# Optimization experiments

Hardware: AMD Instinct MI355X
Metric: run time of the kernel (lower is better)

The kernel has to match this reference:

```python
import jax, jax.numpy as jnp
import numpy as np

B, QH, QW = 16, 64, 64
KH, KW = 64, 64
H, D, DK, K, S = 8, 256, 32, 4, 1


def setup_inputs() -> dict:
    key = jax.random.key(0)
    ks = jax.random.split(key, 16)
    def lin(i, din, dout, wscale=1.0):
        w = jax.random.normal(ks[i], (din, dout), jnp.float32) * (wscale / np.sqrt(din))
        b = jax.random.normal(ks[i + 1], (dout,), jnp.float32) * 0.02
        return w, b
    Wq, bq = lin(0, D, D)
    Wb, bb = lin(2, D, D)
    Wk, bk = lin(4, D, D)
    Woff, boff = lin(6, D, 2 * H * K * S, wscale=0.1)  # small offsets keep samples near ref point
    WA, bA = lin(8, D, H * K * S)
    Wm, bm = lin(10, D, D)
    return dict(
        query=jax.random.normal(ks[12], (B, QH, QW, D), jnp.float32),
        keys=jax.random.normal(ks[13], (B, KH, KW, D), jnp.float32),
        ref_point=jax.random.uniform(ks[14], (B, QH, QW, 2), jnp.float32),
        src_query=jax.random.normal(ks[15], (B, QH, QW, D), jnp.float32),
        Wq=Wq, bq=bq, Wb=Wb, bb=bb, Wk=Wk, bk=bk,
        Woff=Woff, boff=boff, WA=WA, bA=bA, Wm=Wm, bm=bm)


def _bilinear_zeros(img, px, py):
    # img [N, Hs, Ws, C]; px, py pixel coords [N, K, QH, QW]
    # Matches torch F.grid_sample(mode='bilinear', padding_mode='zeros'):
    # each out-of-bounds corner contributes zero.
    N, Hs, Ws, _ = img.shape
    x0 = jnp.floor(px); y0 = jnp.floor(py)
    wx1 = px - x0; wy1 = py - y0
    n = jnp.arange(N)[:, None, None, None]
    def corner(xf, yf, w):
        xi = xf.astype(jnp.int32); yi = yf.astype(jnp.int32)
        valid = (xi >= 0) & (xi < Ws) & (yi >= 0) & (yi < Hs)
        v = img[n, jnp.clip(yi, 0, Hs - 1), jnp.clip(xi, 0, Ws - 1)]
        return v * (w * valid)[..., None]
    return (corner(x0, y0, (1 - wx1) * (1 - wy1)) + corner(x0 + 1, y0, wx1 * (1 - wy1))
            + corner(x0, y0 + 1, (1 - wx1) * wy1) + corner(x0 + 1, y0 + 1, wx1 * wy1))


def reference(query, keys, ref_point, src_query, Wq, bq, Wb, bb, Wk, bk,
              Woff, boff, WA, bA, Wm, bm):
    _ = query @ Wq + bq  # q_proj output is computed but unused in the original forward
    sq = src_query @ Wb + bb
    off = (sq @ Woff + boff).reshape(B, QH, QW, H, S, K, 2)
    off = off.transpose(0, 3, 4, 5, 1, 2, 6).reshape(B * H, S, K, QH, QW, 2)
    A = jax.nn.softmax((sq @ WA + bA).reshape(B, QH, QW, H, S * K), axis=-1)
    A = A.transpose(0, 3, 1, 2, 4).reshape(B * H, QH, QW, S, K)
    # k_proj on the (single-scale) key feature map -> per-head maps [B*H, KH, KW, DK]
    kf = (keys @ Wk + bk).reshape(B, KH, KW, H, DK).transpose(0, 3, 1, 2, 4).reshape(B * H, KH, KW, DK)
    # restore_scale then torch .repeat(h,1,1,1): flat index n -> batch n % B (faithful to original)
    rr = ref_point * jnp.array([KW - 1, KH - 1], jnp.float32)
    rr = jnp.tile(rr, (H, 1, 1, 1))  # [B*H, QH, QW, 2]
    samples = []
    for l in range(S):
        pts = rr[:, None] + off[:, l]                 # [B*H, K, QH, QW, 2]
        vgx = 2.0 * pts[..., 0] / max(KW - 1, 1) - 1.0
        vgy = 2.0 * pts[..., 1] / max(KH - 1, 1) - 1.0
        px = ((vgx + 1.0) * KW - 1.0) / 2.0           # grid_sample align_corners=False unnormalize
        py = ((vgy + 1.0) * KH - 1.0) / 2.0
        samples.append(_bilinear_zeros(kf, px, py))   # [B*H, K, QH, QW, DK]
    samp = jnp.stack(samples, axis=1)                 # [B*H, S, K, QH, QW, DK]
    feat = jnp.einsum('nskhwd,nhwsk->nhwd', samp, A)  # weighted sum over scales*points
    feat = feat.reshape(B, H, QH, QW, DK).transpose(0, 2, 3, 1, 4).reshape(B, QH, QW, D)
    return feat @ Wm + bm
```

## Files before the change

### kernel.cpp

```cpp
#include <hip/hip_runtime.h>
#include <hip/hip_bf16.h>

using bf16 = __hip_bfloat16;
typedef short bf16x8 __attribute__((ext_vector_type(8)));
typedef short s16x4 __attribute__((ext_vector_type(4)));
typedef float f32x4 __attribute__((ext_vector_type(4)));
typedef unsigned int u32x4 __attribute__((ext_vector_type(4)));

#define DD 256
#define MTOT 65536

static __device__ __forceinline__ short f2bs(float f) {
    bf16 h = __float2bfloat16(f);
    return *reinterpret_cast<short*>(&h);
}

static __device__ __forceinline__ void gll16(const void* g, void* l) {
    __builtin_amdgcn_global_load_lds(
        (const __attribute__((address_space(1))) unsigned int*)g,
        (__attribute__((address_space(3))) unsigned int*)l, 16, 0, 0);
}

static __device__ __forceinline__ int swz_idx(int n, int k) {
    return n * 256 + ((((k >> 3) ^ (n & 7)) << 3) | (k & 7));
}

__global__ __launch_bounds__(256) void k_setup(
    const float* __restrict__ Wk, const float* __restrict__ Wm,
    bf16* __restrict__ WkT, bf16* __restrict__ WmT,
    const float* __restrict__ Wb, const float* __restrict__ bb,
    const float* __restrict__ Woff, const float* __restrict__ boff,
    const float* __restrict__ WA, const float* __restrict__ bA,
    bf16* __restrict__ WCt, float* __restrict__ bc)
{
    __shared__ float colw[256];
    __shared__ float red[256];
    int bid = blockIdx.x, t = threadIdx.x;
    if (bid < 512) {
        int idx = bid * 256 + t;
        int which = idx >> 16, e = idx & 65535;
        int i = e >> 8, j = e & 255;
        const float* src = which == 0 ? Wk : Wm;
        bf16*        dst = which == 0 ? WkT : WmT;
        dst[swz_idx(j, i)] = __float2bfloat16(src[e]);
        return;
    }
    int j = bid - 512;
    float cw = (j < 64) ? Woff[t * 64 + j] : WA[t * 32 + (j - 64)];
    colw[t] = cw;
    red[t] = bb[t] * cw;
    __syncthreads();
    float v = 0.f;
    const float* wbrow = Wb + (size_t)t * 256;
#pragma unroll 8
    for (int i = 0; i < 256; ++i) v += wbrow[i] * colw[i];
    WCt[swz_idx(j, t)] = __float2bfloat16(v);
    for (int s = 128; s > 0; s >>= 1) {
        __syncthreads();
        if (t < s) red[t] += red[t + s];
    }
    if (t == 0) bc[j] = red[0] + ((j < 64) ? boff[j] : bA[j - 64]);
}

template <int NTW, int NCOLS>
static __device__ __forceinline__ void gemm_lds3(
    const float* __restrict__ Av, const bf16* __restrict__ BTswz,
    bf16* __restrict__ Bs, char* __restrict__ As,
    int row0, int tid, f32x4 (&acc)[2][NTW])
{
    const int wave = tid >> 6, lane = tid & 63;
    const int rg = wave >> 1, cg = wave & 1;
    const int rsub = lane & 15, kg = lane >> 4;
    constexpr int SB = NCOLS / 32;
    const int arow_l = lane >> 4;
    const int kb  = (lane & 15) * 4;
    const int g_l = (lane & 15) >> 1;
    const int sub = (lane & 15) & 1;

    f32x4 areg[4];
    auto loadA = [&](int s) {
#pragma unroll
        for (int c = 0; c < 4; ++c) {
            int row = wave * 16 + c * 4 + arow_l;
            areg[c] = *(const f32x4*)(Av + (size_t)(row0 + row) * DD + s * 64 + kb);
        }
    };
    auto writeA = [&](int buf) {
#pragma unroll
        for (int c = 0; c < 4; ++c) {
            int row = wave * 16 + c * 4 + arow_l;
            s16x4 p;
#pragma unroll
            for (int e = 0; e < 4; ++e) p[e] = f2bs(areg[c][e]);
            *(s16x4*)(As + buf * 8192 + row * 128 + ((g_l ^ (row & 7)) << 4) + sub * 8) = p;
        }
    };
    auto stageB = [&](int s) {
#pragma unroll
        for (int i = 0; i < SB; ++i) {
            int cc = wave * SB + i;
            int i16 = cc * 64 + lane;
            int n = i16 >> 3, lg = i16 & 7;
            gll16(BTswz + (size_t)n * 256 + s * 64 + lg * 8, (char*)Bs + (size_t)i16 * 16);
        }
    };

    loadA(0);
    asm volatile("s_waitcnt vmcnt(0)" ::: "memory");
    writeA(0);
    int cur = 0;
#pragma unroll
    for (int s = 0; s < 4; ++s) {
        stageB(s);
        __builtin_amdgcn_sched_barrier(0);
        if (s < 3) {
            loadA(s + 1);
            asm volatile("s_waitcnt vmcnt(4)" ::: "memory");
        } else {
            asm volatile("s_waitcnt vmcnt(0)" ::: "memory");
        }
        asm volatile("s_waitcnt lgkmcnt(0)" ::: "memory");
        __builtin_amdgcn_s_barrier();
#pragma unroll
        for (int kkl = 0; kkl < 2; ++kkl) {
            bf16x8 afr[2];
#pragma unroll
            for (int st = 0; st < 2; ++st) {
                int row = rg * 32 + st * 16 + rsub;
                int g = kkl * 4 + kg;
                afr[st] = *(const bf16x8*)(As + cur * 8192 + row * 128 + ((g ^ (row & 7)) << 4));
            }
            int lg = kkl * 4 + kg;
#pragma unroll
            for (int nt = 0; nt < NTW; ++nt) {
                int n = cg * (NTW * 16) + nt * 16 + rsub;
                bf16x8 b = *(const bf16x8*)((const char*)Bs + (size_t)n * 128 + ((lg ^ (n & 7)) << 4));
                acc[0][nt] = __builtin_amdgcn_mfma_f32_16x16x32_bf16(afr[0], b, acc[0][nt], 0, 0, 0);
                acc[1][nt] = __builtin_amdgcn_mfma_f32_16x16x32_bf16(afr[1], b, acc[1][nt], 0, 0, 0);
            }
        }
        if (s < 3) {
            asm volatile("s_waitcnt vmcnt(0)" ::: "memory");
            writeA(cur ^ 1);
        }
        asm volatile("s_waitcnt lgkmcnt(0)" ::: "memory");
        __builtin_amdgcn_s_barrier();
        cur ^= 1;
    }
}

template <int NTW, int NCOLS>
static __device__ __forceinline__ void gemm_lds2b(
    const bf16* __restrict__ Av, const bf16* __restrict__ BTswz,
    bf16* __restrict__ Bs, char* __restrict__ As,
    int row0, int tid, f32x4 (&acc)[2][NTW])
{
    const int wave = tid >> 6, lane = tid & 63;
    const int rg = wave >> 1, cg = wave & 1;
    const int rsub = lane & 15, kg = lane >> 4;
    constexpr int SB = NCOLS / 32;
    constexpr int SA = 2;
    constexpr int ABYTES = 8192;

    auto stageB = [&](int s) {
#pragma unroll
        for (int i = 0; i < SB; ++i) {
            int cc = wave * SB + i;
            int i16 = cc * 64 + lane;
            int n = i16 >> 3, lg = i16 & 7;
            gll16(BTswz + (size_t)n * 256 + s * 64 + lg * 8, (char*)Bs + (size_t)i16 * 16);
        }
    };
    auto stageA = [&](int s, int buf) {
#pragma unroll
        for (int i = 0; i < SA; ++i) {
            int cc = wave * 2 + i;
            int row = cc * 8 + (lane >> 3);
            int g = (lane & 7) ^ (row & 7);
            gll16(Av + (size_t)(row0 + row) * DD + s * 64 + g * 8,
                  As + (size_t)buf * ABYTES + cc * 1024 + lane * 16);
        }
    };

    stageA(0, 0);
    int cur = 0;
#pragma unroll
    for (int s = 0; s < 4; ++s) {
        stageB(s);
        __builtin_amdgcn_sched_barrier(0);
        if (s < 3) {
            stageA(s + 1, cur ^ 1);
            asm volatile("s_waitcnt vmcnt(%0)" :: "i"(SA) : "memory");
        } else {
            asm volatile("s_waitcnt vmcnt(0)" ::: "memory");
        }
        __builtin_amdgcn_s_barrier();
#pragma unroll
        for (int kkl = 0; kkl < 2; ++kkl) {
            bf16x8 afr[2];
#pragma unroll
            for (int st = 0; st < 2; ++st) {
                int row = rg * 32 + st * 16 + rsub;
                const char* base = As + cur * ABYTES + row * 128;
                int g = kkl * 4 + kg;
                afr[st] = *(const bf16x8*)(base + ((g ^ (row & 7)) << 4));
            }
            int lg = kkl * 4 + kg;
#pragma unroll
            for (int nt = 0; nt < NTW; ++nt) {
                int n = cg * (NTW * 16) + nt * 16 + rsub;
                bf16x8 b = *(const bf16x8*)((const char*)Bs + (size_t)n * 128 + ((lg ^ (n & 7)) << 4));
                acc[0][nt] = __builtin_amdgcn_mfma_f32_16x16x32_bf16(afr[0], b, acc[0][nt], 0, 0, 0);
                acc[1][nt] = __builtin_amdgcn_mfma_f32_16x16x32_bf16(afr[1], b, acc[1][nt], 0, 0, 0);
            }
        }
        asm volatile("s_waitcnt lgkmcnt(0)" ::: "memory");
        __builtin_amdgcn_s_barrier();
        cur ^= 1;
    }
}

__global__ __launch_bounds__(256) void k_offA(
    const float* __restrict__ src, const bf16* __restrict__ WCt, const float* __restrict__ bc,
    float* __restrict__ off_ws, float* __restrict__ A_ws)
{
    __shared__ __align__(16) bf16 Bs[96 * 64];
    __shared__ __align__(16) char As[2 * 8192];
    int tid = threadIdx.x, lane = tid & 63, wave = tid >> 6;
    int row0 = blockIdx.x * 64;
    f32x4 acc[2][3] = {};
    gemm_lds3<3, 96>(src, WCt, Bs, As, row0, tid, acc);
    int col = lane & 15;
    int jbase = (wave & 1) * 48;
    int rb = row0 + (wave >> 1) * 32 + ((lane >> 4) << 2);
#pragma unroll
    for (int mt = 0; mt < 2; ++mt) {
#pragma unroll
        for (int nt = 0; nt < 3; ++nt) {
            int j = jbase + nt * 16 + col;
            if (j < 64) {
                float bias = bc[j];
#pragma unroll
                for (int r = 0; r < 4; ++r) {
                    int m = rb + mt * 16 + r;
                    off_ws[(size_t)m * 64 + j] = acc[mt][nt][r] + bias;
                }
            } else {
                int ac = j - 64;
                float bias = bc[j];
#pragma unroll
                for (int r = 0; r < 4; ++r) {
                    int m = rb + mt * 16 + r;
                    float v  = acc[mt][nt][r] + bias;
                    float mx = fmaxf(v, __shfl_xor(v, 1));
                    mx       = fmaxf(mx, __shfl_xor(mx, 2));
                    float e  = __expf(v - mx);
                    float su = e + __shfl_xor(e, 1);
                    su      += __shfl_xor(su, 2);
                    A_ws[(size_t)m * 32 + ac] = e / su;
                }
            }
        }
    }
}

__global__ __launch_bounds__(256) void k_gemm_kf(
    const float* __restrict__ keys, const bf16* __restrict__ WkT,
    const float* __restrict__ bk, bf16* __restrict__ kf)
{
    __shared__ __align__(16) bf16 Bs[256 * 64];
    __shared__ __align__(16) char As[2 * 8192];
    int tid = threadIdx.x, lane = tid & 63, wave = tid >> 6;
    int row0 = blockIdx.x * 64;
    f32x4 acc[2][8] = {};
    gemm_lds3<8, 256>(keys, WkT, Bs, As, row0, tid, acc);
    int col = lane & 15;
    int jbase = (wave & 1) * 128;
    int rb = row0 + (wave >> 1) * 32 + ((lane >> 4) << 2);
#pragma unroll
    for (int mt = 0; mt < 2; ++mt)
#pragma unroll
        for (int nt = 0; nt < 8; ++nt) {
            int j = jbase + nt * 16 + col;
            float bias = bk[j];
#pragma unroll
            for (int r = 0; r < 4; ++r) {
                int m = rb + mt * 16 + r;
                size_t dst = (((size_t)(m >> 12) * 8 + (j >> 5)) * 4096 + (m & 4095)) * 32 + (j & 31);
                kf[dst] = __float2bfloat16(acc[mt][nt][r] + bias);
            }
        }
}

__global__ __launch_bounds__(256) void k_sample(
    const float* __restrict__ ref_point, const float* __restrict__ off_ws,
    const float* __restrict__ A_ws, const bf16* __restrict__ kf,
    bf16* __restrict__ feat, int blk0)
{
    int bid = blockIdx.x + blk0;
    int xcd = bid & 7, within = bid >> 3;
    int b = xcd * 2 + (within >> 9);
    int pixblk = within & 511;
    int t  = threadIdx.x;
    int q  = t >> 5;
    int h  = (t >> 2) & 7;
    int cg = t & 3;
    int m  = (b << 12) + pixblk * 8 + q;
    int pix = m & 4095;
    int rbatch = (b * 8 + h) & 15;
    const float* rp = ref_point + ((size_t)rbatch * 4096 + pix) * 2;
    float rx = rp[0] * 63.0f;
    float ry = rp[1] * 63.0f;
    const bf16* kfh = kf + ((size_t)(b * 8 + h) * 4096) * 32 + cg * 8;
    f32x4 o0 = *(const f32x4*)(off_ws + (size_t)m * 64 + h * 8);
    f32x4 o1 = *(const f32x4*)(off_ws + (size_t)m * 64 + h * 8 + 4);
    f32x4 av = *(const f32x4*)(A_ws  + (size_t)m * 32 + h * 4);
    float acc[8] = {};
#pragma unroll
    for (int k = 0; k < 4; ++k) {
        float ox = (k < 2) ? o0[2 * k] : o1[2 * k - 4];
        float oy = (k < 2) ? o0[2 * k + 1] : o1[2 * k - 3];
        float a  = av[k];
        float px = (rx + ox) * (64.0f / 63.0f) - 0.5f;
        float py = (ry + oy) * (64.0f / 63.0f) - 0.5f;
        float x0 = floorf(px), y0 = floorf(py);
        float wx1 = px - x0, wy1 = py - y0;
        int xi = (int)x0, yi = (int)y0;
        float ax0 = (1.f - wx1) * ((xi     >= 0 && xi     < 64) ? 1.f : 0.f);
        float ax1 = wx1         * ((xi + 1 >= 0 && xi + 1 < 64) ? 1.f : 0.f);
        float ay0 = (1.f - wy1) * ((yi     >= 0 && yi     < 64) ? a : 0.f);
        float ay1 = wy1         * ((yi + 1 >= 0 && yi + 1 < 64) ? a : 0.f);
        int xc0 = min(max(xi, 0), 63),      xc1 = min(max(xi + 1, 0), 63);
        int yc0 = min(max(yi, 0), 63) * 64, yc1 = min(max(yi + 1, 0), 63) * 64;
        float w00 = ax0 * ay0, w01 = ax1 * ay0, w10 = ax0 * ay1, w11 = ax1 * ay1;
        bf16x8 v00 = *(const bf16x8*)(kfh + (yc0 + xc0) * 32);
        bf16x8 v01 = *(const bf16x8*)(kfh + (yc0 + xc1) * 32);
        bf16x8 v10 = *(const bf16x8*)(kfh + (yc1 + xc0) * 32);
        bf16x8 v11 = *(const bf16x8*)(kfh + (yc1 + xc1) * 32);
        u32x4 u00 = __builtin_bit_cast(u32x4, v00);
        u32x4 u01 = __builtin_bit_cast(u32x4, v01);
        u32x4 u10 = __builtin_bit_cast(u32x4, v10);
        u32x4 u11 = __builtin_bit_cast(u32x4, v11);
#pragma unroll
        for (int d = 0; d < 4; ++d) {
            acc[2 * d]     += w00 * __uint_as_float(u00[d] << 16)
                            + w01 * __uint_as_float(u01[d] << 16)
                            + w10 * __uint_as_float(u10[d] << 16)
                            + w11 * __uint_as_float(u11[d] << 16);
            acc[2 * d + 1] += w00 * __uint_as_float(u00[d] & 0xffff0000u)
                            + w01 * __uint_as_float(u01[d] & 0xffff0000u)
                            + w10 * __uint_as_float(u10[d] & 0xffff0000u)
                            + w11 * __uint_as_float(u11[d] & 0xffff0000u);
        }
    }
    bf16x8 o;
#pragma unroll
    for (int e = 0; e < 8; ++e) o[e] = f2bs(acc[e]);
    *(bf16x8*)(feat + (size_t)m * DD + h * 32 + cg * 8) = o;
}

__global__ __launch_bounds__(256) void k_gemm_out(
    const bf16* __restrict__ feat, const bf16* __restrict__ WmT,
    const float* __restrict__ bm, float* __restrict__ out)
{
    __shared__ __align__(16) bf16 Bs[256 * 64];
    __shared__ __align__(16) char As[2 * 8192];
    int tid = threadIdx.x, lane = tid & 63, wave = tid >> 6;
    int row0 = blockIdx.x * 64;
    f32x4 acc[2][8] = {};
    gemm_lds2b<8, 256>(feat, WmT, Bs, As, row0, tid, acc);
    int col = lane & 15;
    int jbase = (wave & 1) * 128;
    int rb = row0 + (wave >> 1) * 32 + ((lane >> 4) << 2);
#pragma unroll
    for (int mt = 0; mt < 2; ++mt)
#pragma unroll
        for (int nt = 0; nt < 8; ++nt) {
            int j = jbase + nt * 16 + col;
            float bias = bm[j];
#pragma unroll
            for (int r = 0; r < 4; ++r)
                out[(size_t)(rb + mt * 16 + r) * DD + j] =
                    acc[mt][nt][r] + bias;
        }
}

extern "C" void kernel_launch(void* const* d_in, const int* in_sizes, int n_in,
                              void* d_out, int out_size, void* d_ws, size_t ws_size,
                              hipStream_t stream)
{
    (void)in_sizes; (void)n_in; (void)out_size; (void)ws_size;
    const float* keys = (const float*)d_in[1];
    const float* refp = (const float*)d_in[2];
    const float* srcq = (const float*)d_in[3];
    const float* Wb   = (const float*)d_in[6];
    const float* bb   = (const float*)d_in[7];
    const float* Wk   = (const float*)d_in[8];
    const float* bk   = (const float*)d_in[9];
    const float* Woff = (const float*)d_in[10];
    const float* boff = (const float*)d_in[11];
    const float* WA   = (const float*)d_in[12];
    const float* bA   = (const float*)d_in[13];
    const float* Wm   = (const float*)d_in[14];
    const float* bm   = (const float*)d_in[15];

    char* ws = (char*)d_ws;
    bf16*  WkT    = (bf16*)(ws + 0);
    bf16*  WmT    = (bf16*)(ws + 131072);
    bf16*  WCt    = (bf16*)(ws + 262144);
    float* bc     = (float*)(ws + 311296);
    bf16*  kf_ws  = (bf16*)(ws + 442368 + 33554432ull);
    bf16*  feat_ws= (bf16*)(ws + 442368 + 2ull * 33554432ull);
    float* off_ws = (float*)(ws + 442368 + 3ull * 33554432ull);
    float* A_ws   = (float*)(ws + 442368 + 3ull * 33554432ull + 16777216ull);

    float* out = (float*)d_out;

    k_setup    <<<608, 256, 0, stream>>>(Wk, Wm, WkT, WmT, Wb, bb, Woff, boff, WA, bA, WCt, bc);
    k_offA     <<<1024, 256, 0, stream>>>(srcq, WCt, bc, off_ws, A_ws);
    k_gemm_kf  <<<1024, 256, 0, stream>>>(keys, WkT, bk, kf_ws);
    k_sample   <<<4096, 256, 0, stream>>>(refp, off_ws, A_ws, kf_ws, feat_ws, 0);
    k_sample   <<<4096, 256, 0, stream>>>(refp, off_ws, A_ws, kf_ws, feat_ws, 4096);
    k_gemm_out <<<1024, 256, 0, stream>>>(feat_ws, WmT, bm, out);
}
```

Before: 119.0 us.

## Double-buffer B tiles in GEMM kernels and merge sample launches

The three GEMM kernels now double-buffer the weight (B) tile in LDS alongside A, prefetching stage s+1 (and A for s+2 in the fp32 path) before computing stage s. This needs only one barrier per k-step and overlaps global loads with MFMA work. LDS use roughly doubles, up to 80KB in the 256-column kernels, which may lower occupancy. The two k_sample launches are also merged into one 8192-block launch to save a launch gap.

```diff
diff --git a/kernel.cpp b/kernel.cpp
--- a/kernel.cpp
+++ b/kernel.cpp
@@ -63,15 +63,16 @@
 }
 
 template <int NTW, int NCOLS>
-static __device__ __forceinline__ void gemm_lds3(
+static __device__ __forceinline__ void gemm_lds4(
     const float* __restrict__ Av, const bf16* __restrict__ BTswz,
-    bf16* __restrict__ Bs, char* __restrict__ As,
+    char* __restrict__ Bsc, char* __restrict__ As,
     int row0, int tid, f32x4 (&acc)[2][NTW])
 {
     const int wave = tid >> 6, lane = tid & 63;
     const int rg = wave >> 1, cg = wave & 1;
     const int rsub = lane & 15, kg = lane >> 4;
     constexpr int SB = NCOLS / 32;
+    constexpr int BBYTES = NCOLS * 64 * 2;
     const int arow_l = lane >> 4;
     const int kb  = (lane & 15) * 4;
     const int g_l = (lane & 15) >> 1;
@@ -95,32 +96,37 @@
             *(s16x4*)(As + buf * 8192 + row * 128 + ((g_l ^ (row & 7)) << 4) + sub * 8) = p;
         }
     };
-    auto stageB = [&](int s) {
+    auto stageB = [&](int s, int buf) {
 #pragma unroll
         for (int i = 0; i < SB; ++i) {
             int cc = wave * SB + i;
             int i16 = cc * 64 + lane;
             int n = i16 >> 3, lg = i16 & 7;
-            gll16(BTswz + (size_t)n * 256 + s * 64 + lg * 8, (char*)Bs + (size_t)i16 * 16);
+            gll16(BTswz + (size_t)n * 256 + s * 64 + lg * 8,
+                  Bsc + buf * BBYTES + (size_t)i16 * 16);
         }
     };
 
     loadA(0);
     asm volatile("s_waitcnt vmcnt(0)" ::: "memory");
     writeA(0);
+    stageB(0, 0);
+    __builtin_amdgcn_sched_barrier(0);
+    loadA(1);
+    asm volatile("s_waitcnt vmcnt(0)" ::: "memory");
+    asm volatile("s_waitcnt lgkmcnt(0)" ::: "memory");
+    __builtin_amdgcn_s_barrier();
+
     int cur = 0;
 #pragma unroll
     for (int s = 0; s < 4; ++s) {
-        stageB(s);
-        __builtin_amdgcn_sched_barrier(0);
         if (s < 3) {
-            loadA(s + 1);
-            asm volatile("s_waitcnt vmcnt(4)" ::: "memory");
-        } else {
-            asm volatile("s_waitcnt vmcnt(0)" ::: "memory");
-        }
-        asm volatile("s_waitcnt lgkmcnt(0)" ::: "memory");
-        __builtin_amdgcn_s_barrier();
+            writeA(cur ^ 1);
+            stageB(s + 1, cur ^ 1);
+            __builtin_amdgcn_sched_barrier(0);
+            if (s < 2) loadA(s + 2);
+            __builtin_amdgcn_sched_barrier(0);
+        }
 #pragma unroll
         for (int kkl = 0; kkl < 2; ++kkl) {
             bf16x8 afr[2];
@@ -134,87 +140,82 @@
 #pragma unroll
             for (int nt = 0; nt < NTW; ++nt) {
                 int n = cg * (NTW * 16) + nt * 16 + rsub;
-                bf16x8 b = *(const bf16x8*)((const char*)Bs + (size_t)n * 128 + ((lg ^ (n & 7)) << 4));
+                bf16x8 b = *(const bf16x8*)(Bsc + cur * BBYTES + (size_t)n * 128 + ((lg ^ (n & 7)) << 4));
                 acc[0][nt] = __builtin_amdgcn_mfma_f32_16x16x32_bf16(afr[0], b, acc[0][nt], 0, 0, 0);
                 acc[1][nt] = __builtin_amdgcn_mfma_f32_16x16x32_bf16(afr[1], b, acc[1][nt], 0, 0, 0);
             }
         }
-        if (s < 3) {
-            asm volatile("s_waitcnt vmcnt(0)" ::: "memory");
-            writeA(cur ^ 1);
-        }
-        asm volatile("s_waitcnt lgkmcnt(0)" ::: "memory");
+        asm volatile("s_waitcnt vmcnt(0) lgkmcnt(0)" ::: "memory");
         __builtin_amdgcn_s_barrier();
         cur ^= 1;
     }
 }
 
 template <int NTW, int NCOLS>
-static __device__ __forceinline__ void gemm_lds2b(
+static __device__ __forceinline__ void gemm_lds5(
     const bf16* __restrict__ Av, const bf16* __restrict__ BTswz,
-    bf16* __restrict__ Bs, char* __restrict__ As,
+    char* __restrict__ Bsc, char* __restrict__ As,
     int row0, int tid, f32x4 (&acc)[2][NTW])
 {
     const int wave = tid >> 6, lane = tid & 63;
     const int rg = wave >> 1, cg = wave & 1;
     const int rsub = lane & 15, kg = lane >> 4;
     constexpr int SB = NCOLS / 32;
-    constexpr int SA = 2;
-    constexpr int ABYTES = 8192;
-
-    auto stageB = [&](int s) {
+    constexpr int BBYTES = NCOLS * 64 * 2;
+
+    auto stageB = [&](int s, int buf) {
 #pragma unroll
         for (int i = 0; i < SB; ++i) {
             int cc = wave * SB + i;
             int i16 = cc * 64 + lane;
             int n = i16 >> 3, lg = i16 & 7;
-            gll16(BTswz + (size_t)n * 256 + s * 64 + lg * 8, (char*)Bs + (size_t)i16 * 16);
+            gll16(BTswz + (size_t)n * 256 + s * 64 + lg * 8,
+                  Bsc + buf * BBYTES + (size_t)i16 * 16);
         }
     };
     auto stageA = [&](int s, int buf) {
 #pragma unroll
-        for (int i = 0; i < SA; ++i) {
+        for (int i = 0; i < 2; ++i) {
             int cc = wave * 2 + i;
             int row = cc * 8 + (lane >> 3);
             int g = (lane & 7) ^ (row & 7);
             gll16(Av + (size_t)(row0 + row) * DD + s * 64 + g * 8,
-                  As + (size_t)buf * ABYTES + cc * 1024 + lane * 16);
+                  As + (size_t)buf * 8192 + cc * 1024 + lane * 16);
         }
     };
 
+    stageB(0, 0);
     stageA(0, 0);
+    asm volatile("s_waitcnt vmcnt(0)" ::: "memory");
+    __builtin_amdgcn_s_barrier();
+
     int cur = 0;
 #pragma unroll
     for (int s = 0; s < 4; ++s) {
-        stageB(s);
-        __builtin_amdgcn_sched_barrier(0);
         if (s < 3) {
+            stageB(s + 1, cur ^ 1);
             stageA(s + 1, cur ^ 1);
-            asm volatile("s_waitcnt vmcnt(%0)" :: "i"(SA) : "memory");
-        } else {
-            asm volatile("s_waitcnt vmcnt(0)" ::: "memory");
-        }
-        __builtin_amdgcn_s_barrier();
+            __builtin_amdgcn_sched_barrier(0);
+        }
 #pragma unroll
         for (int kkl = 0; kkl < 2; ++kkl) {
             bf16x8 afr[2];
 #pragma unroll
             for (int st = 0; st < 2; ++st) {
                 int row = rg * 32 + st * 16 + rsub;
-                const char* base = As + cur * ABYTES + row * 128;
                 int g = kkl * 4 + kg;
-                afr[st] = *(const bf16x8*)(base + ((g ^ (row & 7)) << 4));
+                afr[st] = *(const bf16x8*)(As + cur * 8192 + row * 128 + ((g ^ (row & 7)) << 4));
             }
             int lg = kkl * 4 + kg;
 #pragma unroll
             for (int nt = 0; nt < NTW; ++nt) {
                 int n = cg * (NTW * 16) + nt * 16 + rsub;
-                bf16x8 b = *(const bf16x8*)((const char*)Bs + (size_t)n * 128 + ((lg ^ (n & 7)) << 4));
+                bf16x8 b = *(const bf16x8*)(Bsc + cur * BBYTES + (size_t)n * 128 + ((lg ^ (n & 7)) << 4));
                 acc[0][nt] = __builtin_amdgcn_mfma_f32_16x16x32_bf16(afr[0], b, acc[0][nt], 0, 0, 0);
                 acc[1][nt] = __builtin_amdgcn_mfma_f32_16x16x32_bf16(afr[1], b, acc[1][nt], 0, 0, 0);
             }
         }
-        asm volatile("s_waitcnt lgkmcnt(0)" ::: "memory");
+        asm volatile("s_waitcnt vmcnt(0) lgkmcnt(0)" ::: "memory");
         __builtin_amdgcn_s_barrier();
         cur ^= 1;
     }
@@ -224,12 +225,12 @@
     const float* __restrict__ src, const bf16* __restrict__ WCt, const float* __restrict__ bc,
     float* __restrict__ off_ws, float* __restrict__ A_ws)
 {
-    __shared__ __align__(16) bf16 Bs[96 * 64];
+    __shared__ __align__(16) char Bsc[2 * 12288];
     __shared__ __align__(16) char As[2 * 8192];
     int tid = threadIdx.x, lane = tid & 63, wave = tid >> 6;
     int row0 = blockIdx.x * 64;
     f32x4 acc[2][3] = {};
-    gemm_lds3<3, 96>(src, WCt, Bs, As, row0, tid, acc);
+    gemm_lds4<3, 96>(src, WCt, Bsc, As, row0, tid, acc);
     int col = lane & 15;
     int jbase = (wave & 1) * 48;
     int rb = row0 + (wave >> 1) * 32 + ((lane >> 4) << 2);
@@ -268,12 +269,12 @@
     const float* __restrict__ keys, const bf16* __restrict__ WkT,
     const float* __restrict__ bk, bf16* __restrict__ kf)
 {
-    __shared__ __align__(16) bf16 Bs[256 * 64];
+    __shared__ __align__(16) char Bsc[2 * 32768];
     __shared__ __align__(16) char As[2 * 8192];
     int tid = threadIdx.x, lane = tid & 63, wave = tid >> 6;
     int row0 = blockIdx.x * 64;
     f32x4 acc[2][8] = {};
-    gemm_lds3<8, 256>(keys, WkT, Bs, As, row0, tid, acc);
+    gemm_lds4<8, 256>(keys, WkT, Bsc, As, row0, tid, acc);
     int col = lane & 15;
     int jbase = (wave & 1) * 128;
     int rb = row0 + (wave >> 1) * 32 + ((lane >> 4) << 2);
@@ -295,9 +296,9 @@
 __global__ __launch_bounds__(256) void k_sample(
     const float* __restrict__ ref_point, const float* __restrict__ off_ws,
     const float* __restrict__ A_ws, const bf16* __restrict__ kf,
-    bf16* __restrict__ feat, int blk0)
-{
-    int bid = blockIdx.x + blk0;
+    bf16* __restrict__ feat)
+{
+    int bid = blockIdx.x;
     int xcd = bid & 7, within = bid >> 3;
     int b = xcd * 2 + (within >> 9);
     int pixblk = within & 511;
@@ -363,12 +364,12 @@
     const bf16* __restrict__ feat, const bf16* __restrict__ WmT,
     const float* __restrict__ bm, float* __restrict__ out)
 {
-    __shared__ __align__(16) bf16 Bs[256 * 64];
+    __shared__ __align__(16) char Bsc[2 * 32768];
     __shared__ __align__(16) char As[2 * 8192];
     int tid = threadIdx.x, lane = tid & 63, wave = tid >> 6;
     int row0 = blockIdx.x * 64;
     f32x4 acc[2][8] = {};
-    gemm_lds2b<8, 256>(feat, WmT, Bs, As, row0, tid, acc);
+    gemm_lds5<8, 256>(feat, WmT, Bsc, As, row0, tid, acc);
     int col = lane & 15;
     int jbase = (wave & 1) * 128;
     int rb = row0 + (wave >> 1) * 32 + ((lane >> 4) << 2);
@@ -419,7 +420,6 @@
     k_setup    <<<608, 256, 0, stream>>>(Wk, Wm, WkT, WmT, Wb, bb, Woff, boff, WA, bA, WCt, bc);
     k_offA     <<<1024, 256, 0, stream>>>(srcq, WCt, bc, off_ws, A_ws);
     k_gemm_kf  <<<1024, 256, 0, stream>>>(keys, WkT, bk, kf_ws);
-    k_sample   <<<4096, 256, 0, stream>>>(refp, off_ws, A_ws, kf_ws, feat_ws, 0);
-    k_sample   <<<4096, 256, 0, stream>>>(refp, off_ws, A_ws, kf_ws, feat_ws, 4096);
+    k_sample   <<<8192, 256, 0, stream>>>(refp, off_ws, A_ws, kf_ws, feat_ws);
     k_gemm_out <<<1024, 256, 0, stream>>>(feat_ws, WmT, bm, out);
 }
```

Result: faster. 114.4 us (median of 2 runs) (-3.8%).
